# Optimization experiments

Hardware: AMD Instinct MI355X
Metric: run time of the kernel (lower is better)

Reference implementation:

```python
import jax, jax.numpy as jnp
import numpy as np

N, E, IN, HID, H, L, G = 50000, 500000, 64, 128, 4, 3, 64
C = HID // H


def setup_inputs() -> dict:
    key = jax.random.key(0)
    ks = jax.random.split(key, 24)
    def lin(k, i, o):
        return jax.random.normal(k, (i, o), jnp.float32) * (1.0 / np.sqrt(i))
    d = {}
    d["x"] = jax.random.normal(ks[0], (N, IN), jnp.float32)
    d["edge_index"] = jax.random.randint(ks[1], (2, E), 0, N, jnp.int32)
    d["batch"] = jnp.sort(jax.random.randint(ks[2], (N,), 0, G, jnp.int32))
    # layer 0 (in_dim -> hidden)
    d["l0_Wq"] = lin(ks[3], IN, HID); d["l0_bq"] = jnp.zeros((HID,), jnp.float32)
    d["l0_Wk"] = lin(ks[4], IN, HID); d["l0_bk"] = jnp.zeros((HID,), jnp.float32)
    d["l0_Wv"] = lin(ks[5], IN, HID); d["l0_bv"] = jnp.zeros((HID,), jnp.float32)
    d["l0_Ws"] = lin(ks[6], IN, HID); d["l0_bs"] = jnp.zeros((HID,), jnp.float32)
    d["l0_Wbeta"] = lin(ks[7], 3 * HID, 1)
    d["l0_ln_g"] = jnp.ones((HID,), jnp.float32); d["l0_ln_b"] = jnp.zeros((HID,), jnp.float32)
    # layers 1..L-1 (hidden -> hidden), stacked on leading axis
    M = L - 1
    def slin(k, i, o):
        return jax.random.normal(k, (M, i, o), jnp.float32) * (1.0 / np.sqrt(i))
    d["Wq"] = slin(ks[8], HID, HID); d["bq"] = jnp.zeros((M, HID), jnp.float32)
    d["Wk"] = slin(ks[9], HID, HID); d["bk"] = jnp.zeros((M, HID), jnp.float32)
    d["Wv"] = slin(ks[10], HID, HID); d["bv"] = jnp.zeros((M, HID), jnp.float32)
    d["Ws"] = slin(ks[11], HID, HID); d["bs"] = jnp.zeros((M, HID), jnp.float32)
    d["Wbeta"] = slin(ks[12], 3 * HID, 1)
    d["ln_g"] = jnp.ones((M, HID), jnp.float32); d["ln_b"] = jnp.zeros((M, HID), jnp.float32)
    d["mlp_W1"] = lin(ks[13], HID, HID); d["mlp_b1"] = jnp.zeros((HID,), jnp.float32)
    d["mlp_W2"] = lin(ks[14], HID, 1); d["mlp_b2"] = jnp.zeros((1,), jnp.float32)
    return d


def _conv(x, ei, Wq, bq, Wk, bk, Wv, bv, Ws, bs, Wbeta):
    """PyG TransformerConv with beta=True, concat=True (eval mode, no dropout)."""
    src, dst = ei[0], ei[1]
    q = (x @ Wq + bq).reshape(N, H, C)[dst]   # [E,H,C] target queries
    k = (x @ Wk + bk).reshape(N, H, C)[src]   # [E,H,C] source keys
    v = (x @ Wv + bv).reshape(N, H, C)[src]   # [E,H,C] source values
    alpha = (q * k).sum(-1) / np.sqrt(C)      # [E,H]
    amax = jax.lax.stop_gradient(jax.ops.segment_max(alpha, dst, num_segments=N))
    p = jnp.exp(alpha - amax[dst])
    denom = jax.ops.segment_sum(p, dst, num_segments=N)  # [N,H]
    p = p / denom[dst]                                   # segment softmax per dst node
    out = jax.ops.segment_sum(p[:, :, None] * v, dst, num_segments=N).reshape(N, HID)
    x_r = x @ Ws + bs                                    # root/skip transform
    beta = jax.nn.sigmoid(jnp.concatenate([out, x_r, out - x_r], axis=-1) @ Wbeta)  # [N,1]
    return beta * x_r + (1.0 - beta) * out


def _ln(x, g, b):
    mu = x.mean(-1, keepdims=True)
    var = x.var(-1, keepdims=True)
    return (x - mu) / jnp.sqrt(var + 1e-5) * g + b


def reference(x, edge_index, batch, l0_Wq, l0_bq, l0_Wk, l0_bk, l0_Wv, l0_bv, l0_Ws,
              l0_bs, l0_Wbeta, l0_ln_g, l0_ln_b, Wq, bq, Wk, bk, Wv, bv, Ws, bs,
              Wbeta, ln_g, ln_b, mlp_W1, mlp_b1, mlp_W2, mlp_b2):
    h = _conv(x, edge_index, l0_Wq, l0_bq, l0_Wk, l0_bk, l0_Wv, l0_bv, l0_Ws, l0_bs, l0_Wbeta)
    h = jax.nn.gelu(_ln(h, l0_ln_g, l0_ln_b), approximate=False)
    for i in range(L - 1):
        h = _conv(h, edge_index, Wq[i], bq[i], Wk[i], bk[i], Wv[i], bv[i], Ws[i], bs[i], Wbeta[i])
        h = jax.nn.gelu(_ln(h, ln_g[i], ln_b[i]), approximate=False)
    cnt = jax.ops.segment_sum(jnp.ones((N, 1), h.dtype), batch, num_segments=G)
    g = jax.ops.segment_sum(h, batch, num_segments=G) / jnp.maximum(cnt, 1.0)  # mean pool
    hm = jax.nn.gelu(g @ mlp_W1 + mlp_b1, approximate=False)
    return (hm @ mlp_W2 + mlp_b2).reshape(-1)
```

## Files before the change

### kernel.cpp

```cpp
#include <hip/hip_runtime.h>
#include <hip/hip_bf16.h>
#include <hip/hip_fp16.h>

#define NN 50000
#define EE 500000
#define DIN 64
#define HIDD 128
#define NG 64
#define NB1 49

typedef short short8 __attribute__((ext_vector_type(8)));
typedef float f32x4 __attribute__((ext_vector_type(4)));
typedef _Float16 hf2 __attribute__((ext_vector_type(2)));

#define GLL(g, l)                                                              \
  __builtin_amdgcn_global_load_lds(                                            \
      (const __attribute__((address_space(1))) unsigned*)(g),                  \
      (__attribute__((address_space(3))) unsigned*)(l), 16, 0, 0)

__device__ __forceinline__ unsigned short f2bf(float f) {
  unsigned u = __float_as_uint(f);
  u += 0x7fffu + ((u >> 16) & 1u);
  return (unsigned short)(u >> 16);
}
__device__ __forceinline__ float bfl(unsigned short u) {
  return __uint_as_float((unsigned)u << 16);
}
__device__ __forceinline__ unsigned short f2h(float f) {
  __half h = __float2half(f);
  return *(unsigned short*)&h;
}
__device__ __forceinline__ hf2 u2h2(unsigned u) {
  union { unsigned u; hf2 h; } c; c.u = u; return c.h;
}
__device__ __forceinline__ float dot2h(hf2 a, hf2 b) {
#if __has_builtin(__builtin_amdgcn_fdot2)
  return __builtin_amdgcn_fdot2(a, b, 0.f, false);
#else
  return (float)a.x * (float)b.x + (float)a.y * (float)b.y;
#endif
}

struct BiasW { const float* b[4]; };
struct PrepW { const float* w[12]; };

__global__ __launch_bounds__(256) void count_kernel(const int* __restrict__ ei,
                                                    int* __restrict__ cnt, int E) {
  int e = blockIdx.x * 256 + threadIdx.x;
  if (e < E) atomicAdd(&cnt[ei[E + e]], 1);
}

__global__ __launch_bounds__(1024) void scan1_kernel(const int* __restrict__ cnts,
                                                     int* __restrict__ starts,
                                                     int* __restrict__ btot) {
  __shared__ int sh[1024];
  int t = threadIdx.x;
  int idx = blockIdx.x * 1024 + t;
  int v = (idx < NN) ? cnts[idx] : 0;
  sh[t] = v;
  __syncthreads();
  for (int off = 1; off < 1024; off <<= 1) {
    int add = (t >= off) ? sh[t - off] : 0;
    __syncthreads();
    sh[t] += add;
    __syncthreads();
  }
  if (idx < NN) starts[idx] = sh[t] - v;
  if (t == 1023) btot[blockIdx.x] = sh[1023];
}

__global__ __launch_bounds__(64) void scan2_kernel(const int* __restrict__ btot,
                                                   int* __restrict__ boff,
                                                   int* __restrict__ starts) {
  int t = threadIdx.x;
  int orig = (t < NB1) ? btot[t] : 0;
  int v = orig;
  for (int off = 1; off < 64; off <<= 1) {
    int n_ = __shfl_up(v, off);
    if (t >= off) v += n_;
  }
  if (t < NB1) boff[t] = v - orig;
  if (t == NB1 - 1) starts[NN] = v;
}

__global__ __launch_bounds__(256) void scan3_kernel(int* __restrict__ starts,
                                                    const int* __restrict__ boff,
                                                    int* __restrict__ pos) {
  int i = blockIdx.x * 256 + threadIdx.x;
  if (i < NN) {
    int s = starts[i] + boff[i >> 10];
    starts[i] = s;
    pos[i] = s;
  }
}

__global__ __launch_bounds__(256) void scatter_kernel(const int* __restrict__ ei,
                                                      int* __restrict__ pos,
                                                      int* __restrict__ csr_src, int E) {
  int e = blockIdx.x * 256 + threadIdx.x;
  if (e < 8) csr_src[E + e] = 0;
  if (e < E) {
    int dst = ei[E + e];
    int p = atomicAdd(&pos[dst], 1);
    csr_src[p] = ei[e];
  }
}

__global__ __launch_bounds__(256) void prep_kernel(PrepW pw, short* __restrict__ wT) {
  int o = blockIdx.x * 256 + threadIdx.x;
  if (o >= 163840) return;
  int m, local, K;
  if (o < 32768) { m = o >> 13; local = o & 8191; K = 64; }
  else { int oo = o - 32768; m = 4 + (oo >> 14); local = oo & 16383; K = 128; }
  int col = local / K;
  int off = (local % K) * 2;
  int sw = off ^ ((col & 7) << 4);
  int k = (sw >> 4) * 8 + ((sw & 15) >> 1);
  wT[o] = (short)f2bf(pw.w[m][(size_t)k * 128 + col]);
}

template <int K, bool BF16IN>
__global__ __launch_bounds__(256) void gemm_pair(
    const void* __restrict__ hin, const short* __restrict__ wT, BiasW bw,
    unsigned short* __restrict__ qb, unsigned short* __restrict__ kvb,
    unsigned short* __restrict__ sb, int N) {
  constexpr int RB = 2 * K;
  constexpr int CALLS = (128 * RB) / 4096;
  const float QSC = 0.17677669529663687f;
  __shared__ short bS[2][128 * K];
  const int grp = blockIdx.y;
  const int m0 = grp ? 1 : 0;
  const int m1 = grp ? 2 : 3;
  const int t = threadIdx.x, l = t & 63, wv = t >> 6;

  {
    const char* g0 = (const char*)(wT + (size_t)m0 * 128 * K);
    const char* g1 = (const char*)(wT + (size_t)m1 * 128 * K);
    char* lp0 = (char*)&bS[0][0];
    char* lp1 = (char*)&bS[1][0];
#pragma unroll
    for (int i = 0; i < CALLS; ++i)
      GLL(g0 + i * 4096 + wv * 1024 + l * 16, lp0 + i * 4096 + wv * 1024);
#pragma unroll
    for (int i = 0; i < CALLS; ++i)
      GLL(g1 + i * 4096 + wv * 1024 + l * 16, lp1 + i * 4096 + wv * 1024);
  }
  __syncthreads();

  const int lr = l & 15, lk = l >> 4;
  const float* __restrict__ bias0 = bw.b[m0];
  const float* __restrict__ bias1 = bw.b[m1];

  for (int r0 = blockIdx.x * 64 + wv * 16; r0 < N; r0 += gridDim.x * 64) {
    const int gr = r0 + lr;
    const bool ok = gr < N;
    short8 hfrag[K / 32];
    if (BF16IN) {
      const short* hs = (const short*)hin;
#pragma unroll
      for (int ks = 0; ks < K / 32; ++ks) {
        short8 z = {0, 0, 0, 0, 0, 0, 0, 0};
        hfrag[ks] = ok ? *(const short8*)(hs + (size_t)gr * K + ks * 32 + lk * 8) : z;
      }
    } else {
      const float* hf = (const float*)hin;
#pragma unroll
      for (int ks = 0; ks < K / 32; ++ks) {
        short8 pk = {0, 0, 0, 0, 0, 0, 0, 0};
        if (ok) {
          const float* hp = hf + (size_t)gr * K + ks * 32 + lk * 8;
          f32x4 f0 = *(const f32x4*)hp;
          f32x4 f1 = *(const f32x4*)(hp + 4);
          pk[0] = f2bf(f0.x); pk[1] = f2bf(f0.y); pk[2] = f2bf(f0.z); pk[3] = f2bf(f0.w);
          pk[4] = f2bf(f1.x); pk[5] = f2bf(f1.y); pk[6] = f2bf(f1.z); pk[7] = f2bf(f1.w);
        }
        hfrag[ks] = pk;
      }
    }

    f32x4 accA[8] = {}, accB[8] = {};
#pragma unroll
    for (int ks = 0; ks < K / 32; ++ks) {
#pragma unroll
      for (int cf = 0; cf < 8; ++cf) {
        int col = cf * 16 + lr;
        unsigned bb = col * RB + ((((ks * 4 + lk) * 16)) ^ ((col & 7) << 4));
        short8 w0 = *(const short8*)((const char*)&bS[0][0] + bb);
        short8 w1 = *(const short8*)((const char*)&bS[1][0] + bb);
        accA[cf] = __builtin_amdgcn_mfma_f32_16x16x32_bf16(w0, hfrag[ks], accA[cf], 0, 0, 0);
        accB[cf] = __builtin_amdgcn_mfma_f32_16x16x32_bf16(w1, hfrag[ks], accB[cf], 0, 0, 0);
      }
    }

    if (gr < N) {
#pragma unroll
      for (int cf = 0; cf < 8; ++cf) {
        int ch0 = cf * 16 + lk * 4;
        f32x4 bA = *(const f32x4*)&bias0[ch0];
        f32x4 bB = *(const f32x4*)&bias1[ch0];
        float a0 = accA[cf][0] + bA.x, a1 = accA[cf][1] + bA.y;
        float a2 = accA[cf][2] + bA.z, a3 = accA[cf][3] + bA.w;
        float c0 = accB[cf][0] + bB.x, c1 = accB[cf][1] + bB.y;
        float c2 = accB[cf][2] + bB.z, c3 = accB[cf][3] + bB.w;
        if (grp == 0) {
          ushort4 q;
          q.x = f2h(a0 * QSC); q.y = f2h(a1 * QSC);
          q.z = f2h(a2 * QSC); q.w = f2h(a3 * QSC);
          *(ushort4*)&qb[(size_t)gr * 128 + ch0] = q;
          ushort4 s;
          s.x = f2bf(c0); s.y = f2bf(c1); s.z = f2bf(c2); s.w = f2bf(c3);
          *(ushort4*)&sb[(size_t)gr * 128 + ch0] = s;
        } else {
          uint4 o;
          o.x = (unsigned)f2h(a0) | ((unsigned)f2h(a1) << 16);
          o.y = (unsigned)f2h(c0) | ((unsigned)f2h(c1) << 16);
          o.z = (unsigned)f2h(a2) | ((unsigned)f2h(a3) << 16);
          o.w = (unsigned)f2h(c2) | ((unsigned)f2h(c3) << 16);
          *(uint4*)((unsigned*)kvb + (size_t)gr * 128 + ch0) = o;
        }
      }
    }
  }
}

template <int NB, bool MASK>
__device__ __forceinline__ void att_batch(
    const int* __restrict__ csr, int i, int s1, const unsigned* __restrict__ kvu,
    int lane, hf2 qp, float& d, float& o0, float& o1) {
  int ce = csr[i + (lane & (NB - 1))];
  uint2 w[NB];
#pragma unroll
  for (int e = 0; e < NB; ++e) {
    int s = __builtin_amdgcn_readlane(ce, e);
    w[e] = *((const uint2*)kvu + ((size_t)s << 6) + lane);
  }
#pragma unroll
  for (int e = 0; e < NB; ++e) {
    float part = dot2h(u2h2(w[e].x), qp);
    part += __shfl_xor(part, 1);
    part += __shfl_xor(part, 2);
    part += __shfl_xor(part, 4);
    part += __shfl_xor(part, 8);
    float p = __expf(part);
    if (MASK) p = (i + e < s1) ? p : 0.f;
    d += p;
    __half2 vh = *(__half2*)&w[e].y;
    float2 vf = __half22float2(vh);
    o0 = fmaf(p, vf.x, o0);
    o1 = fmaf(p, vf.y, o1);
  }
}

__global__ __launch_bounds__(256, 8) void attn_fused(
    const unsigned short* __restrict__ qb, const unsigned* __restrict__ kvu,
    const unsigned short* __restrict__ sb, const int* __restrict__ starts,
    const int* __restrict__ csr, const float* __restrict__ Wbeta,
    const float* __restrict__ lng, const float* __restrict__ lnb,
    unsigned short* __restrict__ hout, int N) {
  int wid = (blockIdx.x * 256 + threadIdx.x) >> 6;
  if (wid >= N) return;
  const int lane = threadIdx.x & 63;
  hf2 qp = u2h2(((const unsigned*)qb)[(size_t)wid * 64 + lane]);
  int s0 = starts[wid], s1 = starts[wid + 1];
  float d = 0.f, o0 = 0.f, o1 = 0.f;
  int i = s0;
  for (; i + 8 <= s1; i += 8)
    att_batch<8, false>(csr, i, s1, kvu, lane, qp, d, o0, o1);
  if (i < s1) {
    if (s1 - i <= 4)
      att_batch<4, true>(csr, i, s1, kvu, lane, qp, d, o0, o1);
    else
      att_batch<8, true>(csr, i, s1, kvu, lane, qp, d, o0, o1);
  }
  float inv = d > 0.f ? 1.f / d : 0.f;
  o0 *= inv; o1 *= inv;
  unsigned su = ((const unsigned*)sb)[(size_t)wid * 64 + lane];
  float sx = bfl((unsigned short)su), sy = bfl((unsigned short)(su >> 16));
  float2 wbo = *(const float2*)&Wbeta[2 * lane];
  float2 wbx = *(const float2*)&Wbeta[128 + 2 * lane];
  float2 wbd = *(const float2*)&Wbeta[256 + 2 * lane];
  float bl = o0 * wbo.x + o1 * wbo.y + sx * wbx.x + sy * wbx.y
           + (o0 - sx) * wbd.x + (o1 - sy) * wbd.y;
  bl += __shfl_xor(bl, 1);  bl += __shfl_xor(bl, 2);  bl += __shfl_xor(bl, 4);
  bl += __shfl_xor(bl, 8);  bl += __shfl_xor(bl, 16); bl += __shfl_xor(bl, 32);
  float beta = 1.f / (1.f + __expf(-bl));
  float hx = beta * sx + (1.f - beta) * o0;
  float hy = beta * sy + (1.f - beta) * o1;
  float s = hx + hy, sq = hx * hx + hy * hy;
  s += __shfl_xor(s, 1);  sq += __shfl_xor(sq, 1);
  s += __shfl_xor(s, 2);  sq += __shfl_xor(sq, 2);
  s += __shfl_xor(s, 4);  sq += __shfl_xor(sq, 4);
  s += __shfl_xor(s, 8);  sq += __shfl_xor(sq, 8);
  s += __shfl_xor(s, 16); sq += __shfl_xor(sq, 16);
  s += __shfl_xor(s, 32); sq += __shfl_xor(sq, 32);
  float mu = s * (1.f / 128.f);
  float var = sq * (1.f / 128.f) - mu * mu;
  float rstd = 1.f / sqrtf(var + 1e-5f);
  float2 g2 = *(const float2*)&lng[2 * lane];
  float2 b2 = *(const float2*)&lnb[2 * lane];
  float y0 = (hx - mu) * rstd * g2.x + b2.x;
  float y1 = (hy - mu) * rstd * g2.y + b2.y;
  y0 = 0.5f * y0 * (1.f + erff(y0 * 0.70710678118654752f));
  y1 = 0.5f * y1 * (1.f + erff(y1 * 0.70710678118654752f));
  unsigned outw = (unsigned)f2bf(y0) | ((unsigned)f2bf(y1) << 16);
  ((unsigned*)hout)[(size_t)wid * 64 + lane] = outw;
}

__global__ __launch_bounds__(1024) void pool_mlp_kernel(
    const unsigned short* __restrict__ h, const int* __restrict__ batch,
    const float* __restrict__ W1, const float* __restrict__ b1,
    const float* __restrict__ W2, const float* __restrict__ b2,
    float* __restrict__ out, int N) {
  __shared__ float accS[16][HIDD];
  __shared__ float gS[HIDD];
  __shared__ float red[2];
  const int g = blockIdx.x, t = threadIdx.x;
  int lo, hi;
  {
    int a = 0, b = N;
    while (a < b) { int m = (a + b) >> 1; if (batch[m] < g) a = m + 1; else b = m; }
    lo = a;
    b = N;
    while (a < b) { int m = (a + b) >> 1; if (batch[m] < g + 1) a = m + 1; else b = m; }
    hi = a;
  }
  const unsigned* h32 = (const unsigned*)h;
  const int rg = t >> 6, u = t & 63;
  float a0 = 0.f, a1 = 0.f;
  int n = lo + rg;
  for (; n + 48 < hi; n += 64) {
    unsigned w0 = h32[(size_t)n * 64 + u];
    unsigned w1 = h32[(size_t)(n + 16) * 64 + u];
    unsigned w2 = h32[(size_t)(n + 32) * 64 + u];
    unsigned w3 = h32[(size_t)(n + 48) * 64 + u];
    a0 += bfl((unsigned short)w0) + bfl((unsigned short)w1)
        + bfl((unsigned short)w2) + bfl((unsigned short)w3);
    a1 += bfl((unsigned short)(w0 >> 16)) + bfl((unsigned short)(w1 >> 16))
        + bfl((unsigned short)(w2 >> 16)) + bfl((unsigned short)(w3 >> 16));
  }
  for (; n < hi; n += 16) {
    unsigned w = h32[(size_t)n * 64 + u];
    a0 += bfl((unsigned short)w);
    a1 += bfl((unsigned short)(w >> 16));
  }
  accS[rg][2 * u] = a0;
  accS[rg][2 * u + 1] = a1;
  __syncthreads();
  if (t < HIDD) {
    float s = 0.f;
#pragma unroll
    for (int r = 0; r < 16; ++r) s += accS[r][t];
    gS[t] = s / fmaxf((float)(hi - lo), 1.f);
  }
  __syncthreads();
  if (t < HIDD) {
    float s = b1[t];
#pragma unroll 4
    for (int k = 0; k < HIDD; ++k) s = fmaf(gS[k], W1[k * HIDD + t], s);
    s = 0.5f * s * (1.f + erff(s * 0.70710678118654752f));
    float p = s * W2[t];
    p += __shfl_xor(p, 1);  p += __shfl_xor(p, 2);  p += __shfl_xor(p, 4);
    p += __shfl_xor(p, 8);  p += __shfl_xor(p, 16); p += __shfl_xor(p, 32);
    if ((t & 63) == 0) red[t >> 6] = p;
  }
  __syncthreads();
  if (t == 0) out[g] = red[0] + red[1] + b2[0];
}

extern "C" void kernel_launch(void* const* d_in, const int* in_sizes, int n_in,
                              void* d_out, int out_size, void* d_ws, size_t ws_size,
                              hipStream_t stream) {
  const float* x        = (const float*)d_in[0];
  const int*   ei       = (const int*)d_in[1];
  const int*   batch    = (const int*)d_in[2];
  const float* l0_Wq    = (const float*)d_in[3];
  const float* l0_bq    = (const float*)d_in[4];
  const float* l0_Wk    = (const float*)d_in[5];
  const float* l0_bk    = (const float*)d_in[6];
  const float* l0_Wv    = (const float*)d_in[7];
  const float* l0_bv    = (const float*)d_in[8];
  const float* l0_Ws    = (const float*)d_in[9];
  const float* l0_bs    = (const float*)d_in[10];
  const float* l0_Wbeta = (const float*)d_in[11];
  const float* l0_lng   = (const float*)d_in[12];
  const float* l0_lnb   = (const float*)d_in[13];
  const float* Wq       = (const float*)d_in[14];
  const float* bq       = (const float*)d_in[15];
  const float* Wk       = (const float*)d_in[16];
  const float* bk       = (const float*)d_in[17];
  const float* Wv       = (const float*)d_in[18];
  const float* bv       = (const float*)d_in[19];
  const float* Ws       = (const float*)d_in[20];
  const float* bs       = (const float*)d_in[21];
  const float* Wbeta    = (const float*)d_in[22];
  const float* lng      = (const float*)d_in[23];
  const float* lnb      = (const float*)d_in[24];
  const float* mlp_W1   = (const float*)d_in[25];
  const float* mlp_b1   = (const float*)d_in[26];
  const float* mlp_W2   = (const float*)d_in[27];
  const float* mlp_b2   = (const float*)d_in[28];
  float* outp = (float*)d_out;

  char* ws = (char*)d_ws;
  size_t off = 0;
  auto alloc = [&](size_t bytes) -> void* {
    void* p = ws + off;
    off = (off + bytes + 255) & ~(size_t)255;
    return p;
  };
  unsigned short* h0  = (unsigned short*)alloc((size_t)NN * HIDD * 2);
  unsigned short* h1  = (unsigned short*)alloc((size_t)NN * HIDD * 2);
  unsigned short* qbv = (unsigned short*)alloc((size_t)NN * HIDD * 2);
  unsigned short* sbv = (unsigned short*)alloc((size_t)NN * HIDD * 2);
  unsigned short* kvb = (unsigned short*)alloc((size_t)NN * 256 * 2);
  short*  wT     = (short*)alloc((size_t)163840 * 2);
  int*    starts = (int*)alloc((size_t)(NN + 1) * 4);
  int*    pos    = (int*)alloc((size_t)NN * 4);
  int*    csr    = (int*)alloc((size_t)(EE + 8) * 4);
  int*    btot   = (int*)alloc((size_t)NB1 * 4);
  int*    boff   = (int*)alloc((size_t)NB1 * 4);
  (void)ws_size; (void)in_sizes; (void)n_in; (void)out_size;

  PrepW pw = {{l0_Wq, l0_Wk, l0_Wv, l0_Ws,
               Wq, Wk, Wv, Ws,
               Wq + 16384, Wk + 16384, Wv + 16384, Ws + 16384}};
  prep_kernel<<<640, 256, 0, stream>>>(pw, wT);

  hipMemsetAsync(pos, 0, (size_t)NN * 4, stream);
  count_kernel<<<(EE + 255) / 256, 256, 0, stream>>>(ei, pos, EE);
  scan1_kernel<<<NB1, 1024, 0, stream>>>(pos, starts, btot);
  scan2_kernel<<<1, 64, 0, stream>>>(btot, boff, starts);
  scan3_kernel<<<(NN + 255) / 256, 256, 0, stream>>>(starts, boff, pos);
  scatter_kernel<<<(EE + 255) / 256, 256, 0, stream>>>(ei, pos, csr, EE);

  dim3 ggrid(256, 2);
  int agrid = (NN + 3) / 4;
  const unsigned* kvu = (const unsigned*)kvb;

  BiasW b0 = {{l0_bq, l0_bk, l0_bv, l0_bs}};
  gemm_pair<DIN, false><<<ggrid, 256, 0, stream>>>(x, wT, b0, qbv, kvb, sbv, NN);
  attn_fused<<<agrid, 256, 0, stream>>>(qbv, kvu, sbv, starts, csr, l0_Wbeta,
                                        l0_lng, l0_lnb, h0, NN);

  BiasW b1s = {{bq, bk, bv, bs}};
  gemm_pair<HIDD, true><<<ggrid, 256, 0, stream>>>(h0, wT + 32768, b1s, qbv, kvb, sbv, NN);
  attn_fused<<<agrid, 256, 0, stream>>>(qbv, kvu, sbv, starts, csr, Wbeta,
                                        lng, lnb, h1, NN);

  BiasW b2s = {{bq + HIDD, bk + HIDD, bv + HIDD, bs + HIDD}};
  gemm_pair<HIDD, true><<<ggrid, 256, 0, stream>>>(h1, wT + 98304, b2s, qbv, kvb, sbv, NN);
  attn_fused<<<agrid, 256, 0, stream>>>(qbv, kvu, sbv, starts, csr, Wbeta + 384,
                                        lng + HIDD, lnb + HIDD, h0, NN);

  pool_mlp_kernel<<<NG, 1024, 0, stream>>>(h0, batch, mlp_W1, mlp_b1, mlp_W2,
                                           mlp_b2, outp, NN);
}
```

Baseline: 306.3 us.

## Process four edges per wavefront in parallel lane groups in attention kernel

```diff
diff --git a/kernel.cpp b/kernel.cpp
--- a/kernel.cpp
+++ b/kernel.cpp
@@ -33,11 +33,11 @@
 __device__ __forceinline__ hf2 u2h2(unsigned u) {
   union { unsigned u; hf2 h; } c; c.u = u; return c.h;
 }
-__device__ __forceinline__ float dot2h(hf2 a, hf2 b) {
+__device__ __forceinline__ float dot2a(hf2 a, hf2 b, float c) {
 #if __has_builtin(__builtin_amdgcn_fdot2)
-  return __builtin_amdgcn_fdot2(a, b, 0.f, false);
+  return __builtin_amdgcn_fdot2(a, b, c, false);
 #else
-  return (float)a.x * (float)b.x + (float)a.y * (float)b.y;
+  return c + (float)a.x * (float)b.x + (float)a.y * (float)b.y;
 #endif
 }
 
@@ -223,34 +223,6 @@
   }
 }
 
-template <int NB, bool MASK>
-__device__ __forceinline__ void att_batch(
-    const int* __restrict__ csr, int i, int s1, const unsigned* __restrict__ kvu,
-    int lane, hf2 qp, float& d, float& o0, float& o1) {
-  int ce = csr[i + (lane & (NB - 1))];
-  uint2 w[NB];
-#pragma unroll
-  for (int e = 0; e < NB; ++e) {
-    int s = __builtin_amdgcn_readlane(ce, e);
-    w[e] = *((const uint2*)kvu + ((size_t)s << 6) + lane);
-  }
-#pragma unroll
-  for (int e = 0; e < NB; ++e) {
-    float part = dot2h(u2h2(w[e].x), qp);
-    part += __shfl_xor(part, 1);
-    part += __shfl_xor(part, 2);
-    part += __shfl_xor(part, 4);
-    part += __shfl_xor(part, 8);
-    float p = __expf(part);
-    if (MASK) p = (i + e < s1) ? p : 0.f;
-    d += p;
-    __half2 vh = *(__half2*)&w[e].y;
-    float2 vf = __half22float2(vh);
-    o0 = fmaf(p, vf.x, o0);
-    o1 = fmaf(p, vf.y, o1);
-  }
-}
-
 __global__ __launch_bounds__(256, 8) void attn_fused(
     const unsigned short* __restrict__ qb, const unsigned* __restrict__ kvu,
     const unsigned short* __restrict__ sb, const int* __restrict__ starts,
@@ -259,51 +231,144 @@
     unsigned short* __restrict__ hout, int N) {
   int wid = (blockIdx.x * 256 + threadIdx.x) >> 6;
   if (wid >= N) return;
-  const int lane = threadIdx.x & 63;
-  hf2 qp = u2h2(((const unsigned*)qb)[(size_t)wid * 64 + lane]);
+  const int l = threadIdx.x & 63;
+  const int u = l & 15;
+  const int eg = l >> 4;
+  uint4 qw = *(const uint4*)((const unsigned*)qb + (size_t)wid * 64 + 4 * u);
+  hf2 q0 = u2h2(qw.x), q1 = u2h2(qw.y), q2 = u2h2(qw.z), q3 = u2h2(qw.w);
   int s0 = starts[wid], s1 = starts[wid + 1];
-  float d = 0.f, o0 = 0.f, o1 = 0.f;
+  float d = 0.f;
+  float o0 = 0.f, o1 = 0.f, o2 = 0.f, o3 = 0.f;
+  float o4 = 0.f, o5 = 0.f, o6 = 0.f, o7 = 0.f;
+
+#define EDGE(AA, BB, VALID)                                                    \
+  {                                                                            \
+    float dt = dot2a(u2h2(AA.x), q0,                                           \
+               dot2a(u2h2(AA.z), q1,                                           \
+               dot2a(u2h2(BB.x), q2,                                           \
+               dot2a(u2h2(BB.z), q3, 0.f))));                                  \
+    dt += __shfl_xor(dt, 1);                                                   \
+    dt += __shfl_xor(dt, 2);                                                   \
+    float p = __expf(dt);                                                      \
+    if (!(VALID)) p = 0.f;                                                     \
+    d += p;                                                                    \
+    float2 vf;                                                                 \
+    vf = __half22float2(*(__half2*)&AA.y);                                     \
+    o0 = fmaf(p, vf.x, o0); o1 = fmaf(p, vf.y, o1);                            \
+    vf = __half22float2(*(__half2*)&AA.w);                                     \
+    o2 = fmaf(p, vf.x, o2); o3 = fmaf(p, vf.y, o3);                            \
+    vf = __half22float2(*(__half2*)&BB.y);                                     \
+    o4 = fmaf(p, vf.x, o4); o5 = fmaf(p, vf.y, o5);                            \
+    vf = __half22float2(*(__half2*)&BB.w);                                     \
+    o6 = fmaf(p, vf.x, o6); o7 = fmaf(p, vf.y, o7);                            \
+  }
+
   int i = s0;
-  for (; i + 8 <= s1; i += 8)
-    att_batch<8, false>(csr, i, s1, kvu, lane, qp, d, o0, o1);
-  if (i < s1) {
-    if (s1 - i <= 4)
-      att_batch<4, true>(csr, i, s1, kvu, lane, qp, d, o0, o1);
-    else
-      att_batch<8, true>(csr, i, s1, kvu, lane, qp, d, o0, o1);
-  }
+  for (; i + 8 <= s1; i += 8) {
+    int src0 = csr[i + eg];
+    int src1 = csr[i + 4 + eg];
+    const char* r0 = (const char*)kvu + ((size_t)src0 << 9) + u * 32;
+    const char* r1 = (const char*)kvu + ((size_t)src1 << 9) + u * 32;
+    uint4 A0 = *(const uint4*)r0;
+    uint4 B0 = *(const uint4*)(r0 + 16);
+    uint4 A1 = *(const uint4*)r1;
+    uint4 B1 = *(const uint4*)(r1 + 16);
+    EDGE(A0, B0, true);
+    EDGE(A1, B1, true);
+  }
+  for (; i < s1; i += 4) {
+    int idx = i + eg;
+    bool ok = idx < s1;
+    int src = csr[ok ? idx : s0];
+    const char* r = (const char*)kvu + ((size_t)src << 9) + u * 32;
+    uint4 A = *(const uint4*)r;
+    uint4 B = *(const uint4*)(r + 16);
+    EDGE(A, B, ok);
+  }
+#undef EDGE
+
+  d += __shfl_xor(d, 16); d += __shfl_xor(d, 32);
+  o0 += __shfl_xor(o0, 16); o0 += __shfl_xor(o0, 32);
+  o1 += __shfl_xor(o1, 16); o1 += __shfl_xor(o1, 32);
+  o2 += __shfl_xor(o2, 16); o2 += __shfl_xor(o2, 32);
+  o3 += __shfl_xor(o3, 16); o3 += __shfl_xor(o3, 32);
+  o4 += __shfl_xor(o4, 16); o4 += __shfl_xor(o4, 32);
+  o5 += __shfl_xor(o5, 16); o5 += __shfl_xor(o5, 32);
+  o6 += __shfl_xor(o6, 16); o6 += __shfl_xor(o6, 32);
+  o7 += __shfl_xor(o7, 16); o7 += __shfl_xor(o7, 32);
   float inv = d > 0.f ? 1.f / d : 0.f;
-  o0 *= inv; o1 *= inv;
-  unsigned su = ((const unsigned*)sb)[(size_t)wid * 64 + lane];
-  float sx = bfl((unsigned short)su), sy = bfl((unsigned short)(su >> 16));
-  float2 wbo = *(const float2*)&Wbeta[2 * lane];
-  float2 wbx = *(const float2*)&Wbeta[128 + 2 * lane];
-  float2 wbd = *(const float2*)&Wbeta[256 + 2 * lane];
-  float bl = o0 * wbo.x + o1 * wbo.y + sx * wbx.x + sy * wbx.y
-           + (o0 - sx) * wbd.x + (o1 - sy) * wbd.y;
-  bl += __shfl_xor(bl, 1);  bl += __shfl_xor(bl, 2);  bl += __shfl_xor(bl, 4);
-  bl += __shfl_xor(bl, 8);  bl += __shfl_xor(bl, 16); bl += __shfl_xor(bl, 32);
+  o0 *= inv; o1 *= inv; o2 *= inv; o3 *= inv;
+  o4 *= inv; o5 *= inv; o6 *= inv; o7 *= inv;
+
+  uint4 sw4 = *(const uint4*)((const unsigned*)sb + (size_t)wid * 64 + 4 * u);
+  float s0f = bfl((unsigned short)sw4.x), s1f = bfl((unsigned short)(sw4.x >> 16));
+  float s2f = bfl((unsigned short)sw4.y), s3f = bfl((unsigned short)(sw4.y >> 16));
+  float s4f = bfl((unsigned short)sw4.z), s5f = bfl((unsigned short)(sw4.z >> 16));
+  float s6f = bfl((unsigned short)sw4.w), s7f = bfl((unsigned short)(sw4.w >> 16));
+  f32x4 wo0 = *(const f32x4*)&Wbeta[8 * u];
+  f32x4 wo1 = *(const f32x4*)&Wbeta[8 * u + 4];
+  f32x4 wx0 = *(const f32x4*)&Wbeta[128 + 8 * u];
+  f32x4 wx1 = *(const f32x4*)&Wbeta[128 + 8 * u + 4];
+  f32x4 wd0 = *(const f32x4*)&Wbeta[256 + 8 * u];
+  f32x4 wd1 = *(const f32x4*)&Wbeta[256 + 8 * u + 4];
+  float bl = o0 * wo0.x + o1 * wo0.y + o2 * wo0.z + o3 * wo0.w
+           + o4 * wo1.x + o5 * wo1.y + o6 * wo1.z + o7 * wo1.w
+           + s0f * wx0.x + s1f * wx0.y + s2f * wx0.z + s3f * wx0.w
+           + s4f * wx1.x + s5f * wx1.y + s6f * wx1.z + s7f * wx1.w
+           + (o0 - s0f) * wd0.x + (o1 - s1f) * wd0.y
+           + (o2 - s2f) * wd0.z + (o3 - s3f) * wd0.w
+           + (o4 - s4f) * wd1.x + (o5 - s5f) * wd1.y
+           + (o6 - s6f) * wd1.z + (o7 - s7f) * wd1.w;
+  bl += __shfl_xor(bl, 1); bl += __shfl_xor(bl, 2);
+  bl += __shfl_xor(bl, 4); bl += __shfl_xor(bl, 8);
   float beta = 1.f / (1.f + __expf(-bl));
-  float hx = beta * sx + (1.f - beta) * o0;
-  float hy = beta * sy + (1.f - beta) * o1;
-  float s = hx + hy, sq = hx * hx + hy * hy;
-  s += __shfl_xor(s, 1);  sq += __shfl_xor(sq, 1);
-  s += __shfl_xor(s, 2);  sq += __shfl_xor(sq, 2);
-  s += __shfl_xor(s, 4);  sq += __shfl_xor(sq, 4);
-  s += __shfl_xor(s, 8);  sq += __shfl_xor(sq, 8);
-  s += __shfl_xor(s, 16); sq += __shfl_xor(sq, 16);
-  s += __shfl_xor(s, 32); sq += __shfl_xor(sq, 32);
-  float mu = s * (1.f / 128.f);
+  float h0 = beta * s0f + (1.f - beta) * o0;
+  float h1 = beta * s1f + (1.f - beta) * o1;
+  float h2 = beta * s2f + (1.f - beta) * o2;
+  float h3 = beta * s3f + (1.f - beta) * o3;
+  float h4 = beta * s4f + (1.f - beta) * o4;
+  float h5 = beta * s5f + (1.f - beta) * o5;
+  float h6 = beta * s6f + (1.f - beta) * o6;
+  float h7 = beta * s7f + (1.f - beta) * o7;
+  float sm = h0 + h1 + h2 + h3 + h4 + h5 + h6 + h7;
+  float sq = h0 * h0 + h1 * h1 + h2 * h2 + h3 * h3
+           + h4 * h4 + h5 * h5 + h6 * h6 + h7 * h7;
+  sm += __shfl_xor(sm, 1); sq += __shfl_xor(sq, 1);
+  sm += __shfl_xor(sm, 2); sq += __shfl_xor(sq, 2);
+  sm += __shfl_xor(sm, 4); sq += __shfl_xor(sq, 4);
+  sm += __shfl_xor(sm, 8); sq += __shfl_xor(sq, 8);
+  float mu = sm * (1.f / 128.f);
   float var = sq * (1.f / 128.f) - mu * mu;
   float rstd = 1.f / sqrtf(var + 1e-5f);
-  float2 g2 = *(const float2*)&lng[2 * lane];
-  float2 b2 = *(const float2*)&lnb[2 * lane];
-  float y0 = (hx - mu) * rstd * g2.x + b2.x;
-  float y1 = (hy - mu) * rstd * g2.y + b2.y;
-  y0 = 0.5f * y0 * (1.f + erff(y0 * 0.70710678118654752f));
-  y1 = 0.5f * y1 * (1.f + erff(y1 * 0.70710678118654752f));
-  unsigned outw = (unsigned)f2bf(y0) | ((unsigned)f2bf(y1) << 16);
-  ((unsigned*)hout)[(size_t)wid * 64 + lane] = outw;
+  f32x4 g0 = *(const f32x4*)&lng[8 * u];
+  f32x4 g1 = *(const f32x4*)&lng[8 * u + 4];
+  f32x4 bb0 = *(const f32x4*)&lnb[8 * u];
+  f32x4 bb1 = *(const f32x4*)&lnb[8 * u + 4];
+  const float IS2 = 0.70710678118654752f;
+  float y0 = (h0 - mu) * rstd * g0.x + bb0.x;
+  float y1 = (h1 - mu) * rstd * g0.y + bb0.y;
+  float y2 = (h2 - mu) * rstd * g0.z + bb0.z;
+  float y3 = (h3 - mu) * rstd * g0.w + bb0.w;
+  float y4 = (h4 - mu) * rstd * g1.x + bb1.x;
+  float y5 = (h5 - mu) * rstd * g1.y + bb1.y;
+  float y6 = (h6 - mu) * rstd * g1.z + bb1.z;
+  float y7 = (h7 - mu) * rstd * g1.w + bb1.w;
+  y0 = 0.5f * y0 * (1.f + erff(y0 * IS2));
+  y1 = 0.5f * y1 * (1.f + erff(y1 * IS2));
+  y2 = 0.5f * y2 * (1.f + erff(y2 * IS2));
+  y3 = 0.5f * y3 * (1.f + erff(y3 * IS2));
+  y4 = 0.5f * y4 * (1.f + erff(y4 * IS2));
+  y5 = 0.5f * y5 * (1.f + erff(y5 * IS2));
+  y6 = 0.5f * y6 * (1.f + erff(y6 * IS2));
+  y7 = 0.5f * y7 * (1.f + erff(y7 * IS2));
+  if (eg == 0) {
+    uint4 o;
+    o.x = (unsigned)f2bf(y0) | ((unsigned)f2bf(y1) << 16);
+    o.y = (unsigned)f2bf(y2) | ((unsigned)f2bf(y3) << 16);
+    o.z = (unsigned)f2bf(y4) | ((unsigned)f2bf(y5) << 16);
+    o.w = (unsigned)f2bf(y6) | ((unsigned)f2bf(y7) << 16);
+    *(uint4*)((unsigned*)hout + (size_t)wid * 64 + 4 * u) = o;
+  }
 }
 
 __global__ __launch_bounds__(1024) void pool_mlp_kernel(
```

Measured after the change: 325.4 us. 6.2% more time.
